# Kernel optimization log

Measured on AMD Instinct MI355X. Metric: run time of the kernel, lower is better.

The kernel has to match this reference:

```python
import jax, jax.numpy as jnp
import numpy as np

# Approximate EMD matching (Fan et al. approxmatch): 10 annealed soft-assignment
# rounds with levels -4^j for j = 7..-1 and level 0 for the final round.
_LEVELS = jnp.asarray([-(4.0 ** j) for j in range(7, -2, -1)] + [0.0], dtype=jnp.float32)


def _approx_match(d2, n, m):
    # d2: [b, n, m] squared pairwise distances
    b = d2.shape[0]
    factorl = max(n, m) / float(n)
    factorr = max(n, m) / float(m)
    remainl0 = jnp.full((b, n), factorl, dtype=d2.dtype)
    remainr0 = jnp.full((b, m), factorr, dtype=d2.dtype)
    match0 = jnp.zeros_like(d2)

    def step(carry, level):
        match, remainl, remainr = carry
        w = jnp.exp(level * d2) * remainr[:, None, :]            # [b,n,m]
        w = w / (jnp.sum(w, axis=-1, keepdims=True) + 1e-9)      # row-normalize
        w = w * remainl[:, :, None]                              # scale by left capacity
        ss2 = jnp.sum(w, axis=1)                                 # [b,m] column mass
        s = jnp.minimum(remainr / (ss2 + 1e-9), 1.0)             # column saturation
        w = w * s[:, None, :]
        match = match + w
        remainl = jnp.maximum(remainl - jnp.sum(w, axis=-1), 0.0)
        remainr = jnp.maximum(remainr - jnp.sum(w, axis=1), 0.0)
        return (match, remainl, remainr), None

    (match, _, _), _ = jax.lax.scan(step, (match0, remainl0, remainr0), _LEVELS)
    return match


def setup_inputs() -> dict:
    key = jax.random.key(0)
    k1, k2 = jax.random.split(key)
    xyz1 = jax.random.normal(k1, (16, 2048, 3), dtype=jnp.float32)
    xyz2 = jax.random.normal(k2, (16, 2048, 3), dtype=jnp.float32)
    return {"xyz1": xyz1, "xyz2": xyz2}


def reference(xyz1, xyz2):
    n, m = xyz1.shape[1], xyz2.shape[1]
    diff = xyz1[:, :, None, :] - xyz2[:, None, :, :]             # [b,n,m,3]
    d2 = jnp.sum(diff * diff, axis=-1)                           # [b,n,m]
    match = _approx_match(d2, n, m)
    dist = jnp.sqrt(jnp.maximum(d2, 1e-12))
    cost = jnp.sum(match * dist, axis=(1, 2))                    # [b]
    return cost
```

## Files before the change

### kernel.cpp

```cpp
#include <hip/hip_runtime.h>
#include <math.h>

#define B 16
#define N 2048
#define M 2048
#define BN (B * N)
#define LOG2E 1.4426950408889634f

#define CJ 256
#define NCH (M / CJ)
#define TPB 128
#define RPT 2
#define RBLK (TPB * RPT)

typedef float v2f __attribute__((ext_vector_type(2)));

#define EXP2F(x) __builtin_amdgcn_exp2f(x)
#define SQRTF(x) __builtin_amdgcn_sqrtf(x)

__device__ inline v2f exp2v(v2f a) {
    v2f r;
    r.x = EXP2F(a.x);
    r.y = EXP2F(a.y);
    return r;
}

__global__ __launch_bounds__(256) void k_pack(const float* __restrict__ xyz1,
                                              const float* __restrict__ xyz2,
                                              float4* __restrict__ p1,
                                              float4* __restrict__ p2) {
    int idx = blockIdx.x * 256 + threadIdx.x;
    const float* s = (idx < BN) ? (xyz1 + 3 * (size_t)idx)
                                : (xyz2 + 3 * (size_t)(idx - BN));
    float x = s[0], y = s[1], z = s[2];
    float n = fmaf(x, x, fmaf(y, y, z * z));
    float4 v = make_float4(x, y, z, n);
    if (idx < BN) p1[idx] = v;
    else p2[idx - BN] = v;
}

__global__ __launch_bounds__(256) void k_init(float* __restrict__ rl0,
                                              float* __restrict__ rr0,
                                              float* __restrict__ rs0,
                                              float* __restrict__ rs2,
                                              float* __restrict__ t1b,
                                              float* __restrict__ ss20,
                                              float* __restrict__ cost) {
    int idx = blockIdx.x * 256 + threadIdx.x;
    rl0[idx] = 1.0f;
    rr0[idx] = 1.0f;
    rs0[idx] = 0.0f;
    rs2[idx] = 0.0f;
    t1b[idx] = 0.0f;
    ss20[idx] = 0.0f;
    if (idx < B) cost[idx] = 0.0f;
}

__global__ __launch_bounds__(TPB) void k_rowsum0(const float4* __restrict__ p1,
                                                 const float4* __restrict__ p2,
                                                 float* __restrict__ rs,
                                                 float c2) {
    __shared__ float4 tile4[CJ];
    const int b = blockIdx.z;
    const int tx = threadIdx.x;
    const int i0 = blockIdx.y * RBLK + tx;
    const int i1 = i0 + TPB;

    for (int t = tx; t < CJ; t += TPB) {
        int gj = b * M + blockIdx.x * CJ + t;
        float4 f = p2[gj];
        tile4[t] = make_float4(f.x, f.y, f.z, c2 * f.w);
    }
    __syncthreads();

    float4 fa = p1[b * N + i0];
    float4 fb = p1[b * N + i1];
    const float m2c = -2.0f * c2;
    v2f Xp = {m2c * fa.x, m2c * fb.x};
    v2f Yp = {m2c * fa.y, m2c * fb.y};
    v2f Zp = {m2c * fa.z, m2c * fb.z};
    v2f nip = {c2 * fa.w, c2 * fb.w};

    v2f acc = {0.0f, 0.0f};
#pragma unroll 8
    for (int t = 0; t < CJ; ++t) {
        float4 q4 = tile4[t];
        v2f arg = q4.x * Xp + (q4.y * Yp + (q4.z * Zp + (nip + q4.w)));
        acc += exp2v(arg);
    }
    atomicAdd(&rs[b * N + i0], acc.x);
    atomicAdd(&rs[b * N + i1], acc.y);
}

__global__ __launch_bounds__(TPB) void k_colsum(const float4* __restrict__ p1,
                                                const float4* __restrict__ p2,
                                                const float* __restrict__ rl_in,
                                                float* __restrict__ rl_out,
                                                const float* __restrict__ rs_prev,
                                                const float* __restrict__ rs_cur,
                                                float* __restrict__ rs_zero,
                                                const float* __restrict__ t1_in,
                                                float* __restrict__ t1_zero,
                                                const float* __restrict__ rr,
                                                float* __restrict__ ss2_acc,
                                                float cS) {
    __shared__ float4 tile4[CJ];
    __shared__ float tileA[CJ];
    const int b = blockIdx.z;
    const int tx = threadIdx.x;
    const int j0 = blockIdx.y * RBLK + tx;
    const int j1 = j0 + TPB;

    for (int t = tx; t < CJ; t += TPB) {
        int gi = b * N + blockIdx.x * CJ + t;
        float4 f = p1[gi];
        float rlo = rl_in[gi];
        float ap = rlo / (rs_prev[gi] + 1e-9f);
        float rln = fmaxf(rlo - ap * t1_in[gi], 0.0f);
        float a = rln / (rs_cur[gi] + 1e-9f);
        tile4[t] = make_float4(f.x, f.y, f.z, cS * f.w);
        tileA[t] = a;
        if (blockIdx.y == 0) {
            rl_out[gi] = rln;
            t1_zero[gi] = 0.0f;
            rs_zero[gi] = 0.0f;
        }
    }
    __syncthreads();

    const int gj0 = b * M + j0;
    const int gj1 = b * M + j1;
    float4 fa = p2[gj0];
    float4 fb = p2[gj1];
    const float m2c = -2.0f * cS;
    v2f Xp = {m2c * fa.x, m2c * fb.x};
    v2f Yp = {m2c * fa.y, m2c * fb.y};
    v2f Zp = {m2c * fa.z, m2c * fb.z};
    v2f njp = {cS * fa.w, cS * fb.w};

    v2f acc = {0.0f, 0.0f};
#pragma unroll 8
    for (int t = 0; t < CJ; ++t) {
        float4 q4 = tile4[t];
        v2f arg = q4.x * Xp + (q4.y * Yp + (q4.z * Zp + (njp + q4.w)));
        acc += exp2v(arg) * tileA[t];
    }
    atomicAdd(&ss2_acc[gj0], acc.x * rr[gj0]);
    atomicAdd(&ss2_acc[gj1], acc.y * rr[gj1]);
}

__global__ __launch_bounds__(256) void k_suma(const float* __restrict__ rl_in,
                                              float* __restrict__ rl_out,
                                              const float* __restrict__ rs_prev,
                                              const float* __restrict__ rs_cur,
                                              const float* __restrict__ t1_in,
                                              float* __restrict__ S) {
    __shared__ float red[4];
    const int b = blockIdx.x;
    const int tx = threadIdx.x;
    float s = 0.0f;
#pragma unroll
    for (int k = 0; k < N / 256; ++k) {
        int gi = b * N + k * 256 + tx;
        float rlo = rl_in[gi];
        float ap = rlo / (rs_prev[gi] + 1e-9f);
        float rln = fmaxf(rlo - ap * t1_in[gi], 0.0f);
        rl_out[gi] = rln;
        s += rln / (rs_cur[gi] + 1e-9f);
    }
#pragma unroll
    for (int off = 32; off > 0; off >>= 1)
        s += __shfl_down(s, off, 64);
    if ((tx & 63) == 0) red[tx >> 6] = s;
    __syncthreads();
    if (tx == 0) S[b] = red[0] + red[1] + red[2] + red[3];
}

__global__ __launch_bounds__(256) void k_mulss2(const float* __restrict__ rr,
                                                const float* __restrict__ S,
                                                float* __restrict__ ss2_out) {
    int idx = blockIdx.x * 256 + threadIdx.x;
    ss2_out[idx] = rr[idx] * S[idx >> 11];
}

template <int MODE>
__global__ __launch_bounds__(TPB) void k_fused(const float4* __restrict__ p1,
                                               const float4* __restrict__ p2,
                                               const float* __restrict__ rr_in,
                                               float* __restrict__ rr_out,
                                               const float* __restrict__ ss2_in,
                                               float* __restrict__ ss2_zero,
                                               const float* __restrict__ rl_new,
                                               const float* __restrict__ rs_cur,
                                               float* __restrict__ rs_next,
                                               float* __restrict__ t1_acc,
                                               float* __restrict__ cost,
                                               float cS, float invS) {
    __shared__ float4 tile4[CJ];
    __shared__ float2 tile2[CJ];
    const int b = blockIdx.z;
    const int tx = threadIdx.x;
    const int i0 = blockIdx.y * RBLK + tx;
    const int i1 = i0 + TPB;

    for (int t = tx; t < CJ; t += TPB) {
        int gj = b * M + blockIdx.x * CJ + t;
        float4 f = p2[gj];
        float rrv = rr_in[gj];
        float sv = ss2_in[gj];
        float s = fminf(rrv / (sv + 1e-9f), 1.0f);
        float q = rrv * s;
        float rrn = fmaxf(rrv - sv * s, 0.0f);
        tile4[t] = make_float4(f.x, f.y, f.z, q);
        tile2[t] = make_float2(rrn, cS * f.w);
        if (MODE != 2 && blockIdx.y == 0) {
            rr_out[gj] = rrn;
            ss2_zero[gj] = 0.0f;
        }
    }
    __syncthreads();

    float4 fa = p1[b * N + i0];
    float4 fb = p1[b * N + i1];
    const float m2c = -2.0f * cS;
    v2f Xp = {m2c * fa.x, m2c * fb.x};
    v2f Yp = {m2c * fa.y, m2c * fb.y};
    v2f Zp = {m2c * fa.z, m2c * fb.z};
    v2f nip = {cS * fa.w, cS * fb.w};

    v2f T1 = {0.0f, 0.0f}, T2 = {0.0f, 0.0f}, rs = {0.0f, 0.0f};
#pragma unroll 8
    for (int t = 0; t < CJ; ++t) {
        float4 q4 = tile4[t];
        float2 rn = tile2[t];
        v2f arg = q4.x * Xp + (q4.y * Yp + (q4.z * Zp + (nip + rn.y)));
        v2f el, en;
        if (MODE == 0) {
            en = exp2v(arg);
            v2f e2 = en * en;
            el = e2 * e2;
        } else if (MODE == 1) {
            el = exp2v(arg);
        }
        v2f d2 = arg * invS;
        d2.x = fmaxf(d2.x, 1e-12f);
        d2.y = fmaxf(d2.y, 1e-12f);
        v2f sd;
        sd.x = SQRTF(d2.x);
        sd.y = SQRTF(d2.y);
        v2f wq;
        if (MODE == 2) {
            wq.x = q4.w;
            wq.y = q4.w;
        } else {
            wq = el * q4.w;
        }
        T1 += wq;
        T2 += wq * sd;
        if (MODE == 0)
            rs += en * rn.x;
        else if (MODE == 1)
            rs += rn.x;
    }

    const int gi0 = b * N + i0;
    const int gi1 = b * N + i1;
    if (MODE != 2) {
        atomicAdd(&t1_acc[gi0], T1.x);
        atomicAdd(&t1_acc[gi1], T1.y);
        atomicAdd(&rs_next[gi0], rs.x);
        atomicAdd(&rs_next[gi1], rs.y);
    }

    float aa = rl_new[gi0] / (rs_cur[gi0] + 1e-9f);
    float ab = rl_new[gi1] / (rs_cur[gi1] + 1e-9f);
    float contrib = fmaf(aa, T2.x, ab * T2.y);
#pragma unroll
    for (int off = 32; off > 0; off >>= 1)
        contrib += __shfl_down(contrib, off, 64);
    if ((threadIdx.x & 63) == 0) atomicAdd(&cost[b], contrib);
}

extern "C" void kernel_launch(void* const* d_in, const int* in_sizes, int n_in,
                              void* d_out, int out_size, void* d_ws, size_t ws_size,
                              hipStream_t stream) {
    const float* xyz1 = (const float*)d_in[0];
    const float* xyz2 = (const float*)d_in[1];
    float* cost = (float*)d_out;

    float* ws = (float*)d_ws;
    float* rl[2] = {ws + 0 * BN, ws + 1 * BN};
    float* rr[2] = {ws + 2 * BN, ws + 3 * BN};
    float* rs[3] = {ws + 4 * BN, ws + 5 * BN, ws + 6 * BN};
    float* ss2b[2] = {ws + 7 * BN, ws + 8 * BN};
    float* t1[2] = {ws + 9 * BN, ws + 10 * BN};
    float4* p1 = (float4*)(ws + 11 * BN);
    float4* p2 = (float4*)(ws + 15 * BN);
    float* S = ws + 19 * BN;

    static const float levels[10] = {-16384.0f, -4096.0f, -1024.0f, -256.0f,
                                     -64.0f,    -16.0f,   -4.0f,    -1.0f,
                                     -0.25f,    0.0f};
    float c2[10];
    for (int l = 0; l < 10; ++l) c2[l] = levels[l] * LOG2E;

    dim3 grid(NCH, N / RBLK, B);
    dim3 blk(TPB);

    k_pack<<<dim3(2 * BN / 256), dim3(256), 0, stream>>>(xyz1, xyz2, p1, p2);
    k_init<<<dim3(BN / 256), dim3(256), 0, stream>>>(rl[0], rr[0], rs[0], rs[2],
                                                     t1[1], ss2b[0], cost);
    k_rowsum0<<<grid, blk, 0, stream>>>(p1, p2, rs[0], c2[0]);

    for (int l = 0; l < 10; ++l) {
        int p = l & 1;
        if (l < 9) {
            k_colsum<<<grid, blk, 0, stream>>>(
                p1, p2, rl[p], rl[1 - p], rs[(l + 2) % 3], rs[l % 3],
                rs[(l + 1) % 3], t1[1 - p], t1[p], rr[p], ss2b[p], c2[l]);
        } else {
            k_suma<<<dim3(B), dim3(256), 0, stream>>>(
                rl[p], rl[1 - p], rs[(l + 2) % 3], rs[l % 3], t1[1 - p], S);
            k_mulss2<<<dim3(BN / 256), dim3(256), 0, stream>>>(rr[p], S, ss2b[p]);
        }

        if (l <= 7) {
            float cS = c2[l + 1];
            k_fused<0><<<grid, blk, 0, stream>>>(
                p1, p2, rr[p], rr[1 - p], ss2b[p], ss2b[1 - p], rl[1 - p],
                rs[l % 3], rs[(l + 1) % 3], t1[p], cost, cS, 1.0f / cS);
        } else if (l == 8) {
            float cS = c2[8];
            k_fused<1><<<grid, blk, 0, stream>>>(
                p1, p2, rr[p], rr[1 - p], ss2b[p], ss2b[1 - p], rl[1 - p],
                rs[l % 3], rs[(l + 1) % 3], t1[p], cost, cS, 1.0f / cS);
        } else {
            k_fused<2><<<grid, blk, 0, stream>>>(
                p1, p2, rr[p], rr[1 - p], ss2b[p], ss2b[1 - p], rl[1 - p],
                rs[l % 3], rs[(l + 1) % 3], t1[p], cost, 1.0f, 1.0f);
        }
    }
}
```

Before: 646.3 us.

## Retile to 256-thread blocks with smaller chunks and hoist distance scaling out of loop

Halves the column chunk (CJ 128) and doubles threads per block (256), with an occupancy hint in launch_bounds. Replaces the packed v2f arithmetic with scalar fma chains. In the fused kernel it takes sqrt(|arg|) directly and applies one per-launch 1/sqrt(|cS|) factor after the reduction, dropping a per-element multiply and clamp. The smaller chunk doubles the atomic traffic per output, and fabs instead of the 1e-12 clamp changes the numerics slightly near zero distance.

```diff
diff --git a/kernel.cpp b/kernel.cpp
--- a/kernel.cpp
+++ b/kernel.cpp
@@ -7,23 +7,14 @@
 #define BN (B * N)
 #define LOG2E 1.4426950408889634f
 
-#define CJ 256
+#define CJ 128
 #define NCH (M / CJ)
-#define TPB 128
+#define TPB 256
 #define RPT 2
 #define RBLK (TPB * RPT)
 
-typedef float v2f __attribute__((ext_vector_type(2)));
-
 #define EXP2F(x) __builtin_amdgcn_exp2f(x)
 #define SQRTF(x) __builtin_amdgcn_sqrtf(x)
-
-__device__ inline v2f exp2v(v2f a) {
-    v2f r;
-    r.x = EXP2F(a.x);
-    r.y = EXP2F(a.y);
-    return r;
-}
 
 __global__ __launch_bounds__(256) void k_pack(const float* __restrict__ xyz1,
                                               const float* __restrict__ xyz2,
@@ -56,54 +47,54 @@
     if (idx < B) cost[idx] = 0.0f;
 }
 
-__global__ __launch_bounds__(TPB) void k_rowsum0(const float4* __restrict__ p1,
-                                                 const float4* __restrict__ p2,
-                                                 float* __restrict__ rs,
-                                                 float c2) {
+__global__ __launch_bounds__(TPB, 4) void k_rowsum0(const float4* __restrict__ p1,
+                                                    const float4* __restrict__ p2,
+                                                    float* __restrict__ rs,
+                                                    float c2) {
     __shared__ float4 tile4[CJ];
     const int b = blockIdx.z;
     const int tx = threadIdx.x;
     const int i0 = blockIdx.y * RBLK + tx;
     const int i1 = i0 + TPB;
 
-    for (int t = tx; t < CJ; t += TPB) {
-        int gj = b * M + blockIdx.x * CJ + t;
+    if (tx < CJ) {
+        int gj = b * M + blockIdx.x * CJ + tx;
         float4 f = p2[gj];
-        tile4[t] = make_float4(f.x, f.y, f.z, c2 * f.w);
+        tile4[tx] = make_float4(f.x, f.y, f.z, c2 * f.w);
     }
     __syncthreads();
 
     float4 fa = p1[b * N + i0];
     float4 fb = p1[b * N + i1];
     const float m2c = -2.0f * c2;
-    v2f Xp = {m2c * fa.x, m2c * fb.x};
-    v2f Yp = {m2c * fa.y, m2c * fb.y};
-    v2f Zp = {m2c * fa.z, m2c * fb.z};
-    v2f nip = {c2 * fa.w, c2 * fb.w};
-
-    v2f acc = {0.0f, 0.0f};
+    const float Xa = m2c * fa.x, Ya = m2c * fa.y, Za = m2c * fa.z, na = c2 * fa.w;
+    const float Xb = m2c * fb.x, Yb = m2c * fb.y, Zb = m2c * fb.z, nb = c2 * fb.w;
+
+    float acca = 0.0f, accb = 0.0f;
 #pragma unroll 8
     for (int t = 0; t < CJ; ++t) {
         float4 q4 = tile4[t];
-        v2f arg = q4.x * Xp + (q4.y * Yp + (q4.z * Zp + (nip + q4.w)));
-        acc += exp2v(arg);
-    }
-    atomicAdd(&rs[b * N + i0], acc.x);
-    atomicAdd(&rs[b * N + i1], acc.y);
-}
-
-__global__ __launch_bounds__(TPB) void k_colsum(const float4* __restrict__ p1,
-                                                const float4* __restrict__ p2,
-                                                const float* __restrict__ rl_in,
-                                                float* __restrict__ rl_out,
-                                                const float* __restrict__ rs_prev,
-                                                const float* __restrict__ rs_cur,
-                                                float* __restrict__ rs_zero,
-                                                const float* __restrict__ t1_in,
-                                                float* __restrict__ t1_zero,
-                                                const float* __restrict__ rr,
-                                                float* __restrict__ ss2_acc,
-                                                float cS) {
+        float arga = fmaf(q4.x, Xa, fmaf(q4.y, Ya, fmaf(q4.z, Za, na + q4.w)));
+        float argb = fmaf(q4.x, Xb, fmaf(q4.y, Yb, fmaf(q4.z, Zb, nb + q4.w)));
+        acca += EXP2F(arga);
+        accb += EXP2F(argb);
+    }
+    atomicAdd(&rs[b * N + i0], acca);
+    atomicAdd(&rs[b * N + i1], accb);
+}
+
+__global__ __launch_bounds__(TPB, 4) void k_colsum(const float4* __restrict__ p1,
+                                                   const float4* __restrict__ p2,
+                                                   const float* __restrict__ rl_in,
+                                                   float* __restrict__ rl_out,
+                                                   const float* __restrict__ rs_prev,
+                                                   const float* __restrict__ rs_cur,
+                                                   float* __restrict__ rs_zero,
+                                                   const float* __restrict__ t1_in,
+                                                   float* __restrict__ t1_zero,
+                                                   const float* __restrict__ rr,
+                                                   float* __restrict__ ss2_acc,
+                                                   float cS) {
     __shared__ float4 tile4[CJ];
     __shared__ float tileA[CJ];
     const int b = blockIdx.z;
@@ -111,15 +102,15 @@
     const int j0 = blockIdx.y * RBLK + tx;
     const int j1 = j0 + TPB;
 
-    for (int t = tx; t < CJ; t += TPB) {
-        int gi = b * N + blockIdx.x * CJ + t;
+    if (tx < CJ) {
+        int gi = b * N + blockIdx.x * CJ + tx;
         float4 f = p1[gi];
         float rlo = rl_in[gi];
         float ap = rlo / (rs_prev[gi] + 1e-9f);
         float rln = fmaxf(rlo - ap * t1_in[gi], 0.0f);
         float a = rln / (rs_cur[gi] + 1e-9f);
-        tile4[t] = make_float4(f.x, f.y, f.z, cS * f.w);
-        tileA[t] = a;
+        tile4[tx] = make_float4(f.x, f.y, f.z, cS * f.w);
+        tileA[tx] = a;
         if (blockIdx.y == 0) {
             rl_out[gi] = rln;
             t1_zero[gi] = 0.0f;
@@ -128,25 +119,24 @@
     }
     __syncthreads();
 
-    const int gj0 = b * M + j0;
-    const int gj1 = b * M + j1;
-    float4 fa = p2[gj0];
-    float4 fb = p2[gj1];
+    float4 fa = p2[b * M + j0];
+    float4 fb = p2[b * M + j1];
     const float m2c = -2.0f * cS;
-    v2f Xp = {m2c * fa.x, m2c * fb.x};
-    v2f Yp = {m2c * fa.y, m2c * fb.y};
-    v2f Zp = {m2c * fa.z, m2c * fb.z};
-    v2f njp = {cS * fa.w, cS * fb.w};
-
-    v2f acc = {0.0f, 0.0f};
+    const float Xa = m2c * fa.x, Ya = m2c * fa.y, Za = m2c * fa.z, na = cS * fa.w;
+    const float Xb = m2c * fb.x, Yb = m2c * fb.y, Zb = m2c * fb.z, nb = cS * fb.w;
+
+    float acca = 0.0f, accb = 0.0f;
 #pragma unroll 8
     for (int t = 0; t < CJ; ++t) {
         float4 q4 = tile4[t];
-        v2f arg = q4.x * Xp + (q4.y * Yp + (q4.z * Zp + (njp + q4.w)));
-        acc += exp2v(arg) * tileA[t];
-    }
-    atomicAdd(&ss2_acc[gj0], acc.x * rr[gj0]);
-    atomicAdd(&ss2_acc[gj1], acc.y * rr[gj1]);
+        float av = tileA[t];
+        float arga = fmaf(q4.x, Xa, fmaf(q4.y, Ya, fmaf(q4.z, Za, na + q4.w)));
+        float argb = fmaf(q4.x, Xb, fmaf(q4.y, Yb, fmaf(q4.z, Zb, nb + q4.w)));
+        acca = fmaf(EXP2F(arga), av, acca);
+        accb = fmaf(EXP2F(argb), av, accb);
+    }
+    atomicAdd(&ss2_acc[b * M + j0], acca * rr[b * M + j0]);
+    atomicAdd(&ss2_acc[b * M + j1], accb * rr[b * M + j1]);
 }
 
 __global__ __launch_bounds__(256) void k_suma(const float* __restrict__ rl_in,
@@ -184,18 +174,18 @@
 }
 
 template <int MODE>
-__global__ __launch_bounds__(TPB) void k_fused(const float4* __restrict__ p1,
-                                               const float4* __restrict__ p2,
-                                               const float* __restrict__ rr_in,
-                                               float* __restrict__ rr_out,
-                                               const float* __restrict__ ss2_in,
-                                               float* __restrict__ ss2_zero,
-                                               const float* __restrict__ rl_new,
-                                               const float* __restrict__ rs_cur,
-                                               float* __restrict__ rs_next,
-                                               float* __restrict__ t1_acc,
-                                               float* __restrict__ cost,
-                                               float cS, float invS) {
+__global__ __launch_bounds__(TPB, 4) void k_fused(const float4* __restrict__ p1,
+                                                  const float4* __restrict__ p2,
+                                                  const float* __restrict__ rr_in,
+                                                  float* __restrict__ rr_out,
+                                                  const float* __restrict__ ss2_in,
+                                                  float* __restrict__ ss2_zero,
+                                                  const float* __restrict__ rl_new,
+                                                  const float* __restrict__ rs_cur,
+                                                  float* __restrict__ rs_next,
+                                                  float* __restrict__ t1_acc,
+                                                  float* __restrict__ cost,
+                                                  float cS, float rsq) {
     __shared__ float4 tile4[CJ];
     __shared__ float2 tile2[CJ];
     const int b = blockIdx.z;
@@ -203,16 +193,16 @@
     const int i0 = blockIdx.y * RBLK + tx;
     const int i1 = i0 + TPB;
 
-    for (int t = tx; t < CJ; t += TPB) {
-        int gj = b * M + blockIdx.x * CJ + t;
+    if (tx < CJ) {
+        int gj = b * M + blockIdx.x * CJ + tx;
         float4 f = p2[gj];
         float rrv = rr_in[gj];
         float sv = ss2_in[gj];
         float s = fminf(rrv / (sv + 1e-9f), 1.0f);
         float q = rrv * s;
         float rrn = fmaxf(rrv - sv * s, 0.0f);
-        tile4[t] = make_float4(f.x, f.y, f.z, q);
-        tile2[t] = make_float2(rrn, cS * f.w);
+        tile4[tx] = make_float4(f.x, f.y, f.z, q);
+        tile2[tx] = make_float2(rrn, cS * f.w);
         if (MODE != 2 && blockIdx.y == 0) {
             rr_out[gj] = rrn;
             ss2_zero[gj] = 0.0f;
@@ -223,62 +213,59 @@
     float4 fa = p1[b * N + i0];
     float4 fb = p1[b * N + i1];
     const float m2c = -2.0f * cS;
-    v2f Xp = {m2c * fa.x, m2c * fb.x};
-    v2f Yp = {m2c * fa.y, m2c * fb.y};
-    v2f Zp = {m2c * fa.z, m2c * fb.z};
-    v2f nip = {cS * fa.w, cS * fb.w};
-
-    v2f T1 = {0.0f, 0.0f}, T2 = {0.0f, 0.0f}, rs = {0.0f, 0.0f};
+    const float Xa = m2c * fa.x, Ya = m2c * fa.y, Za = m2c * fa.z, na = cS * fa.w;
+    const float Xb = m2c * fb.x, Yb = m2c * fb.y, Zb = m2c * fb.z, nb = cS * fb.w;
+
+    float T1a = 0.0f, T2a = 0.0f, rsa = 0.0f;
+    float T1b = 0.0f, T2b = 0.0f, rsb = 0.0f;
 #pragma unroll 8
     for (int t = 0; t < CJ; ++t) {
         float4 q4 = tile4[t];
         float2 rn = tile2[t];
-        v2f arg = q4.x * Xp + (q4.y * Yp + (q4.z * Zp + (nip + rn.y)));
-        v2f el, en;
+        float arga = fmaf(q4.x, Xa, fmaf(q4.y, Ya, fmaf(q4.z, Za, na + rn.y)));
+        float argb = fmaf(q4.x, Xb, fmaf(q4.y, Yb, fmaf(q4.z, Zb, nb + rn.y)));
+        float sda = SQRTF(fabsf(arga));
+        float sdb = SQRTF(fabsf(argb));
+        float wqa, wqb;
         if (MODE == 0) {
-            en = exp2v(arg);
-            v2f e2 = en * en;
-            el = e2 * e2;
+            float ena = EXP2F(arga);
+            float enb = EXP2F(argb);
+            float e2a = ena * ena, e2b = enb * enb;
+            wqa = (e2a * e2a) * q4.w;
+            wqb = (e2b * e2b) * q4.w;
+            rsa = fmaf(ena, rn.x, rsa);
+            rsb = fmaf(enb, rn.x, rsb);
         } else if (MODE == 1) {
-            el = exp2v(arg);
-        }
-        v2f d2 = arg * invS;
-        d2.x = fmaxf(d2.x, 1e-12f);
-        d2.y = fmaxf(d2.y, 1e-12f);
-        v2f sd;
-        sd.x = SQRTF(d2.x);
-        sd.y = SQRTF(d2.y);
-        v2f wq;
-        if (MODE == 2) {
-            wq.x = q4.w;
-            wq.y = q4.w;
+            wqa = EXP2F(arga) * q4.w;
+            wqb = EXP2F(argb) * q4.w;
+            rsa += rn.x;
+            rsb += rn.x;
         } else {
-            wq = el * q4.w;
-        }
-        T1 += wq;
-        T2 += wq * sd;
-        if (MODE == 0)
-            rs += en * rn.x;
-        else if (MODE == 1)
-            rs += rn.x;
+            wqa = q4.w;
+            wqb = q4.w;
+        }
+        T1a += wqa;
+        T1b += wqb;
+        T2a = fmaf(wqa, sda, T2a);
+        T2b = fmaf(wqb, sdb, T2b);
     }
 
     const int gi0 = b * N + i0;
     const int gi1 = b * N + i1;
     if (MODE != 2) {
-        atomicAdd(&t1_acc[gi0], T1.x);
-        atomicAdd(&t1_acc[gi1], T1.y);
-        atomicAdd(&rs_next[gi0], rs.x);
-        atomicAdd(&rs_next[gi1], rs.y);
+        atomicAdd(&t1_acc[gi0], T1a);
+        atomicAdd(&t1_acc[gi1], T1b);
+        atomicAdd(&rs_next[gi0], rsa);
+        atomicAdd(&rs_next[gi1], rsb);
     }
 
     float aa = rl_new[gi0] / (rs_cur[gi0] + 1e-9f);
     float ab = rl_new[gi1] / (rs_cur[gi1] + 1e-9f);
-    float contrib = fmaf(aa, T2.x, ab * T2.y);
+    float contrib = rsq * fmaf(aa, T2a, ab * T2b);
 #pragma unroll
     for (int off = 32; off > 0; off >>= 1)
         contrib += __shfl_down(contrib, off, 64);
-    if ((threadIdx.x & 63) == 0) atomicAdd(&cost[b], contrib);
+    if ((tx & 63) == 0) atomicAdd(&cost[b], contrib);
 }
 
 extern "C" void kernel_launch(void* const* d_in, const int* in_sizes, int n_in,
@@ -306,10 +293,11 @@
 
     dim3 grid(NCH, N / RBLK, B);
     dim3 blk(TPB);
-
-    k_pack<<<dim3(2 * BN / 256), dim3(256), 0, stream>>>(xyz1, xyz2, p1, p2);
-    k_init<<<dim3(BN / 256), dim3(256), 0, stream>>>(rl[0], rr[0], rs[0], rs[2],
-                                                     t1[1], ss2b[0], cost);
+    dim3 gs(BN / 256);
+    dim3 b256(256);
+
+    k_pack<<<dim3(2 * BN / 256), b256, 0, stream>>>(xyz1, xyz2, p1, p2);
+    k_init<<<gs, b256, 0, stream>>>(rl[0], rr[0], rs[0], rs[2], t1[1], ss2b[0], cost);
     k_rowsum0<<<grid, blk, 0, stream>>>(p1, p2, rs[0], c2[0]);
 
     for (int l = 0; l < 10; ++l) {
@@ -319,21 +307,23 @@
                 p1, p2, rl[p], rl[1 - p], rs[(l + 2) % 3], rs[l % 3],
                 rs[(l + 1) % 3], t1[1 - p], t1[p], rr[p], ss2b[p], c2[l]);
         } else {
-            k_suma<<<dim3(B), dim3(256), 0, stream>>>(
+            k_suma<<<dim3(B), b256, 0, stream>>>(
                 rl[p], rl[1 - p], rs[(l + 2) % 3], rs[l % 3], t1[1 - p], S);
-            k_mulss2<<<dim3(BN / 256), dim3(256), 0, stream>>>(rr[p], S, ss2b[p]);
+            k_mulss2<<<gs, b256, 0, stream>>>(rr[p], S, ss2b[p]);
         }
 
         if (l <= 7) {
             float cS = c2[l + 1];
+            float rsq = 1.0f / sqrtf(fabsf(cS));
             k_fused<0><<<grid, blk, 0, stream>>>(
                 p1, p2, rr[p], rr[1 - p], ss2b[p], ss2b[1 - p], rl[1 - p],
-                rs[l % 3], rs[(l + 1) % 3], t1[p], cost, cS, 1.0f / cS);
+                rs[l % 3], rs[(l + 1) % 3], t1[p], cost, cS, rsq);
         } else if (l == 8) {
             float cS = c2[8];
+            float rsq = 1.0f / sqrtf(fabsf(cS));
             k_fused<1><<<grid, blk, 0, stream>>>(
                 p1, p2, rr[p], rr[1 - p], ss2b[p], ss2b[1 - p], rl[1 - p],
-                rs[l % 3], rs[(l + 1) % 3], t1[p], cost, cS, 1.0f / cS);
+                rs[l % 3], rs[(l + 1) % 3], t1[p], cost, cS, rsq);
         } else {
             k_fused<2><<<grid, blk, 0, stream>>>(
                 p1, p2, rr[p], rr[1 - p], ss2b[p], ss2b[1 - p], rl[1 - p],
```

Result: slower. 838.0 us (+29.7%).
